# Kernel tuning notes

Measured on AMD Instinct MI355X. Metric: run time of the kernel, lower is better.

The kernel has to match this reference:

```python
import jax, jax.numpy as jnp
import numpy as np

B, S, E = 2, 2048, 1024
H, NQ = 16, 8          # n_heads, n_qubits
D = E // H             # head_dim


def setup_inputs() -> dict:
    key = jax.random.key(0)
    ks = jax.random.split(key, 11)
    sc = 0.02
    return {
        "query": jax.random.normal(ks[0], (B, S, E), jnp.float32),
        "key":   jax.random.normal(ks[1], (B, S, E), jnp.float32),
        "value": jax.random.normal(ks[2], (B, S, E), jnp.float32),
        "Wq": jax.random.normal(ks[3], (E, NQ), jnp.float32) * sc,
        "bq": jnp.zeros((NQ,), jnp.float32),
        "Wk": jax.random.normal(ks[4], (E, NQ), jnp.float32) * sc,
        "bk": jnp.zeros((NQ,), jnp.float32),
        "Wv": jax.random.normal(ks[5], (E, E), jnp.float32) * sc,
        "bv": jnp.zeros((E,), jnp.float32),
        "Wo": jax.random.normal(ks[6], (E, E), jnp.float32) * sc,
        "bo": jnp.zeros((E,), jnp.float32),
    }


def reference(query, key, value, Wq, bq, Wk, bk, Wv, bv, Wo, bo):
    # Linear encoders (q/k are computed in the original but, because
    # _apply_rotation is the identity, they never influence the scores).
    q = query @ Wq + bq            # [B,S,NQ] (dead math, kept for fidelity)
    k = key @ Wk + bk              # [B,S,NQ]
    v = value @ Wv + bv            # [B,S,E]
    v = v.reshape(B, S, H, D).transpose(0, 2, 1, 3)  # [B,H,S,D]

    # Quantum overlap: both encoded states are always |0>, so
    # |<q_state|k_state>|^2 == 1 for every (b,i,j) pair.
    scores = jnp.full((B, H, S, S), 1.0 / np.sqrt(NQ), dtype=query.dtype)
    attn = jax.nn.softmax(scores, axis=-1)           # uniform 1/S weights

    out = jnp.einsum('bhij,bhjd->bhid', attn, v)     # [B,H,S,D]
    out = out.transpose(0, 2, 1, 3).reshape(B, S, E)
    out = out @ Wo + bo
    return out, attn
```

## Files before the change

### kernel.cpp

```cpp
#include <hip/hip_runtime.h>

#define B_ 2
#define S_ 2048
#define E_ 1024


typedef float floatx4 __attribute__((ext_vector_type(4)));

__global__ void colsum_partial(const float* __restrict__ value,
                               float* __restrict__ part) {
    int bx  = blockIdx.x;
    int b   = bx >> 7;
    int sp  = bx & 127;
    int tid = threadIdx.x;
    const floatx4* v4 = (const floatx4*)value;
    floatx4 acc = (floatx4)0.0f;
    int rowbase = b * S_ + sp * 16;
    #pragma unroll
    for (int r = 0; r < 16; ++r) {
        acc += v4[(size_t)(rowbase + r) * (E_ / 4) + tid];
    }
    ((floatx4*)part)[(size_t)(b * 128 + sp) * (E_ / 4) + tid] = acc;
}

__global__ void finish_vbar(const float* __restrict__ part,
                            float* __restrict__ vbar) {
    int t = blockIdx.x * 256 + threadIdx.x;
    int b = t >> 10, e = t & 1023;
    float s = 0.f;
    for (int sp = 0; sp < 128; ++sp)
        s += part[(size_t)(b * 128 + sp) * E_ + e];
    vbar[t] = s * (1.0f / (float)S_);
}

__global__ void mv_partial(const float* __restrict__ x,
                           const float* __restrict__ W,
                           float* __restrict__ part) {
    int bx  = blockIdx.x;
    int b   = bx >> 5, ks = bx & 31;
    int tid = threadIdx.x;
    const floatx4* W4 = (const floatx4*)W;
    floatx4 acc = (floatx4)0.0f;
    int k0 = ks * 32;
    #pragma unroll 8
    for (int kk = 0; kk < 32; ++kk) {
        float s  = x[b * E_ + k0 + kk];
        acc += s * W4[(size_t)(k0 + kk) * (E_ / 4) + tid];
    }
    ((floatx4*)part)[(size_t)(b * 32 + ks) * (E_ / 4) + tid] = acc;
}

__global__ void finish_mv(const float* __restrict__ part,
                          const float* __restrict__ bias,
                          float* __restrict__ y) {
    int t = blockIdx.x * 256 + threadIdx.x;
    int b = t >> 10, e = t & 1023;
    float s = bias[e];
    for (int sp = 0; sp < 32; ++sp)
        s += part[(size_t)(b * 32 + sp) * E_ + e];
    y[t] = s;
}

__global__ void fill_out(const float* __restrict__ outrow,
                         float* __restrict__ out) {
    const long long OUT0_4 = 1048576;
    const long long TOT4   = 34603008;
    floatx4* o4 = (floatx4*)out;
    const float A = 1.0f / 2048.0f;
    floatx4 av = (floatx4)A;
    long long stride = (long long)gridDim.x * blockDim.x;
    for (long long i = (long long)blockIdx.x * blockDim.x + threadIdx.x;
         i < TOT4; i += stride) {
        floatx4 w;
        if (i < OUT0_4) {
            int b  = (int)(i >> 19);
            int e4 = (int)(i & 255);
            w = ((const floatx4*)outrow)[b * 256 + e4];
        } else {
            w = av;
        }
        __builtin_nontemporal_store(w, &o4[i]);
    }
}

extern "C" void kernel_launch(void* const* d_in, const int* in_sizes, int n_in,
                              void* d_out, int out_size, void* d_ws, size_t ws_size,
                              hipStream_t stream) {
    const float* value = (const float*)d_in[2];
    const float* Wv    = (const float*)d_in[7];
    const float* bv    = (const float*)d_in[8];
    const float* Wo    = (const float*)d_in[9];
    const float* bo    = (const float*)d_in[10];
    float* out = (float*)d_out;

    float* ws     = (float*)d_ws;
    float* part1  = ws;
    float* vbar   = part1 + 262144;
    float* t1p    = vbar  + 2048;
    float* vbar2  = t1p   + 65536;
    float* t2p    = vbar2 + 2048;
    float* outrow = t2p   + 65536;

    colsum_partial<<<256, 256, 0, stream>>>(value, part1);
    finish_vbar  <<<  8, 256, 0, stream>>>(part1, vbar);
    mv_partial   <<< 64, 256, 0, stream>>>(vbar,  Wv, t1p);
    finish_mv    <<<  8, 256, 0, stream>>>(t1p,   bv, vbar2);
    mv_partial   <<< 64, 256, 0, stream>>>(vbar2, Wo, t2p);
    finish_mv    <<<  8, 256, 0, stream>>>(t2p,   bo, outrow);
    fill_out     <<<2048,256, 0, stream>>>(outrow, out);
}
```

Before: 127.4 us.

## Fuse reduction stages and overlap attention fill with the dependent chain

Cuts seven launches to four. Each finish/reduce step is folded into the next stage's prologue through shared-memory partial sums. The large constant attention-matrix fill is split into four chunks, and each chunk is carried as extra blocks inside one of the small dependent kernels, so those serial stages hide behind bandwidth-bound stores. This removes launch gaps and idle-GPU time during the tiny matvec stages, but the finish reductions are now done redundantly per block.

```diff
diff --git a/kernel.cpp b/kernel.cpp
--- a/kernel.cpp
+++ b/kernel.cpp
@@ -1,85 +1,141 @@
 #include <hip/hip_runtime.h>
-
-#define B_ 2
-#define S_ 2048
-#define E_ 1024
 
 
 typedef float floatx4 __attribute__((ext_vector_type(4)));
 
-__global__ void colsum_partial(const float* __restrict__ value,
-                               float* __restrict__ part) {
-    int bx  = blockIdx.x;
-    int b   = bx >> 7;
-    int sp  = bx & 127;
-    int tid = threadIdx.x;
-    const floatx4* v4 = (const floatx4*)value;
-    floatx4 acc = (floatx4)0.0f;
-    int rowbase = b * S_ + sp * 16;
+#define ATTN_BASE4 1048576LL
+#define CHUNK4     8388608LL
+#define FILLB      2048
+
+__device__ __forceinline__ void fill_chunk(float* __restrict__ out,
+                                           int fb, long long chunk_base) {
+    floatx4* o4 = (floatx4*)out;
+    const floatx4 av = (floatx4)(1.0f / 2048.0f);
+    long long base = chunk_base + (long long)fb * 4096 + threadIdx.x;
     #pragma unroll
-    for (int r = 0; r < 16; ++r) {
-        acc += v4[(size_t)(rowbase + r) * (E_ / 4) + tid];
-    }
-    ((floatx4*)part)[(size_t)(b * 128 + sp) * (E_ / 4) + tid] = acc;
+    for (int it = 0; it < 16; ++it)
+        __builtin_nontemporal_store(av, &o4[base + it * 256]);
 }
 
-__global__ void finish_vbar(const float* __restrict__ part,
-                            float* __restrict__ vbar) {
-    int t = blockIdx.x * 256 + threadIdx.x;
-    int b = t >> 10, e = t & 1023;
-    float s = 0.f;
-    for (int sp = 0; sp < 128; ++sp)
-        s += part[(size_t)(b * 128 + sp) * E_ + e];
-    vbar[t] = s * (1.0f / (float)S_);
+__global__ void k1_colsum_fill(const float* __restrict__ value,
+                               float* __restrict__ part1,
+                               float* __restrict__ out) {
+    int blk = blockIdx.x;
+    if (blk < 256) {
+        int b  = blk >> 7, sp = blk & 127, tid = threadIdx.x;
+        const floatx4* v4 = (const floatx4*)value;
+        floatx4 acc = (floatx4)0.0f;
+        int rowbase = b * 2048 + sp * 16;
+        #pragma unroll
+        for (int r = 0; r < 16; ++r)
+            acc += v4[(size_t)(rowbase + r) * 256 + tid];
+        ((floatx4*)part1)[(size_t)(b * 128 + sp) * 256 + tid] = acc;
+    } else {
+        fill_chunk(out, blk - 256, ATTN_BASE4 + 0 * CHUNK4);
+    }
 }
 
-__global__ void mv_partial(const float* __restrict__ x,
-                           const float* __restrict__ W,
-                           float* __restrict__ part) {
-    int bx  = blockIdx.x;
-    int b   = bx >> 5, ks = bx & 31;
-    int tid = threadIdx.x;
-    const floatx4* W4 = (const floatx4*)W;
-    floatx4 acc = (floatx4)0.0f;
-    int k0 = ks * 32;
-    #pragma unroll 8
-    for (int kk = 0; kk < 32; ++kk) {
-        float s  = x[b * E_ + k0 + kk];
-        acc += s * W4[(size_t)(k0 + kk) * (E_ / 4) + tid];
+__global__ void k2_mv1_fill(const float* __restrict__ part1,
+                            const float* __restrict__ Wv,
+                            float* __restrict__ t1p,
+                            float* __restrict__ out) {
+    int blk = blockIdx.x;
+    if (blk < 64) {
+        __shared__ float red[256];
+        __shared__ float vbar[32];
+        int t = threadIdx.x;
+        int b = blk >> 5, ks = blk & 31, k0 = ks * 32;
+        int kl = t >> 3, seg = t & 7;
+        float s = 0.f;
+        #pragma unroll
+        for (int i = 0; i < 16; ++i) {
+            int sp = seg * 16 + i;
+            s += part1[(size_t)(b * 128 + sp) * 1024 + k0 + kl];
+        }
+        red[t] = s;
+        __syncthreads();
+        if (t < 32) {
+            float v = 0.f;
+            #pragma unroll
+            for (int j = 0; j < 8; ++j) v += red[t * 8 + j];
+            vbar[t] = v * (1.0f / 2048.0f);
+        }
+        __syncthreads();
+        const floatx4* W4 = (const floatx4*)Wv;
+        floatx4 acc = (floatx4)0.0f;
+        #pragma unroll 8
+        for (int kk = 0; kk < 32; ++kk)
+            acc += vbar[kk] * W4[(size_t)(k0 + kk) * 256 + t];
+        ((floatx4*)t1p)[(size_t)(b * 32 + ks) * 256 + t] = acc;
+    } else {
+        fill_chunk(out, blk - 64, ATTN_BASE4 + 1 * CHUNK4);
     }
-    ((floatx4*)part)[(size_t)(b * 32 + ks) * (E_ / 4) + tid] = acc;
 }
 
-__global__ void finish_mv(const float* __restrict__ part,
-                          const float* __restrict__ bias,
-                          float* __restrict__ y) {
-    int t = blockIdx.x * 256 + threadIdx.x;
-    int b = t >> 10, e = t & 1023;
-    float s = bias[e];
-    for (int sp = 0; sp < 32; ++sp)
-        s += part[(size_t)(b * 32 + sp) * E_ + e];
-    y[t] = s;
+__global__ void k3_mv2_fill(const float* __restrict__ t1p,
+                            const float* __restrict__ bv,
+                            const float* __restrict__ Wo,
+                            float* __restrict__ t2p,
+                            float* __restrict__ out) {
+    int blk = blockIdx.x;
+    if (blk < 64) {
+        __shared__ float red[256];
+        __shared__ float vbar2[32];
+        int t = threadIdx.x;
+        int b = blk >> 5, ks = blk & 31, k0 = ks * 32;
+        int kl = t >> 3, seg = t & 7;
+        float s = 0.f;
+        #pragma unroll
+        for (int i = 0; i < 4; ++i) {
+            int sp = seg * 4 + i;
+            s += t1p[(size_t)(b * 32 + sp) * 1024 + k0 + kl];
+        }
+        red[t] = s;
+        __syncthreads();
+        if (t < 32) {
+            float v = bv[k0 + t];
+            #pragma unroll
+            for (int j = 0; j < 8; ++j) v += red[t * 8 + j];
+            vbar2[t] = v;
+        }
+        __syncthreads();
+        const floatx4* W4 = (const floatx4*)Wo;
+        floatx4 acc = (floatx4)0.0f;
+        #pragma unroll 8
+        for (int kk = 0; kk < 32; ++kk)
+            acc += vbar2[kk] * W4[(size_t)(k0 + kk) * 256 + t];
+        ((floatx4*)t2p)[(size_t)(b * 32 + ks) * 256 + t] = acc;
+    } else {
+        fill_chunk(out, blk - 64, ATTN_BASE4 + 2 * CHUNK4);
+    }
 }
 
-__global__ void fill_out(const float* __restrict__ outrow,
-                         float* __restrict__ out) {
-    const long long OUT0_4 = 1048576;
-    const long long TOT4   = 34603008;
-    floatx4* o4 = (floatx4*)out;
-    const float A = 1.0f / 2048.0f;
-    floatx4 av = (floatx4)A;
-    long long stride = (long long)gridDim.x * blockDim.x;
-    for (long long i = (long long)blockIdx.x * blockDim.x + threadIdx.x;
-         i < TOT4; i += stride) {
-        floatx4 w;
-        if (i < OUT0_4) {
-            int b  = (int)(i >> 19);
-            int e4 = (int)(i & 255);
-            w = ((const floatx4*)outrow)[b * 256 + e4];
-        } else {
-            w = av;
+__global__ void k4_bcast_fill(const float* __restrict__ t2p,
+                              const float* __restrict__ bo,
+                              float* __restrict__ out) {
+    int blk = blockIdx.x;
+    if (blk < 64) {
+        __shared__ __align__(16) float orow[1024];
+        int t = threadIdx.x;
+        int b = blk >> 5, rg = blk & 31;
+        int r0 = rg * 64;
+        #pragma unroll
+        for (int cc = 0; cc < 4; ++cc) {
+            int col = cc * 256 + t;
+            float s = bo[col];
+            for (int sp = 0; sp < 32; ++sp)
+                s += t2p[(size_t)(b * 32 + sp) * 1024 + col];
+            orow[col] = s;
         }
-        __builtin_nontemporal_store(w, &o4[i]);
+        __syncthreads();
+        floatx4 w = ((const floatx4*)orow)[t];
+        floatx4* o4 = (floatx4*)out;
+        size_t rowbase = ((size_t)b * 2048 + r0) * 256;
+        #pragma unroll 4
+        for (int r = 0; r < 64; ++r)
+            __builtin_nontemporal_store(w, &o4[rowbase + (size_t)r * 256 + t]);
+    } else {
+        fill_chunk(out, blk - 64, ATTN_BASE4 + 3 * CHUNK4);
     }
 }
 
@@ -93,19 +149,13 @@
     const float* bo    = (const float*)d_in[10];
     float* out = (float*)d_out;
 
-    float* ws     = (float*)d_ws;
-    float* part1  = ws;
-    float* vbar   = part1 + 262144;
-    float* t1p    = vbar  + 2048;
-    float* vbar2  = t1p   + 65536;
-    float* t2p    = vbar2 + 2048;
-    float* outrow = t2p   + 65536;
+    float* ws    = (float*)d_ws;
+    float* part1 = ws;
+    float* t1p   = part1 + 262144;
+    float* t2p   = t1p   + 65536;
 
-    colsum_partial<<<256, 256, 0, stream>>>(value, part1);
-    finish_vbar  <<<  8, 256, 0, stream>>>(part1, vbar);
-    mv_partial   <<< 64, 256, 0, stream>>>(vbar,  Wv, t1p);
-    finish_mv    <<<  8, 256, 0, stream>>>(t1p,   bv, vbar2);
-    mv_partial   <<< 64, 256, 0, stream>>>(vbar2, Wo, t2p);
-    finish_mv    <<<  8, 256, 0, stream>>>(t2p,   bo, outrow);
-    fill_out     <<<2048,256, 0, stream>>>(outrow, out);
+    k1_colsum_fill<<<256 + FILLB, 256, 0, stream>>>(value, part1, out);
+    k2_mv1_fill   <<< 64 + FILLB, 256, 0, stream>>>(part1, Wv, t1p, out);
+    k3_mv2_fill   <<< 64 + FILLB, 256, 0, stream>>>(t1p, bv, Wo, t2p, out);
+    k4_bcast_fill <<< 64 + FILLB, 256, 0, stream>>>(t2p, bo, out);
 }
```

Measured after the change: 109.0 us. -14.5%, faster.

## Fuse seven launches into two kernels, overlapping the attention fill with compute

Applied to the files above, without the earlier changes.

Replaces the seven-kernel chain with two launches. The constant attention-map fill is spread across extra blocks in both kernels, so it overlaps with the column-sum and the matrix-vector work. The two matrix-vector products and their reductions are merged into one kernel that keeps intermediates in shared memory. Each of its 64 blocks redundantly recomputes the full Wv and Wo products for one batch, so the weights are re-read many times, though mostly from cache. This trades extra redundant compute for fewer launches and no separate reduction passes.

```diff
diff --git a/kernel.cpp b/kernel.cpp
--- a/kernel.cpp
+++ b/kernel.cpp
@@ -1,85 +1,91 @@
 #include <hip/hip_runtime.h>
-
-#define B_ 2
-#define S_ 2048
-#define E_ 1024
 
 
 typedef float floatx4 __attribute__((ext_vector_type(4)));
 
-__global__ void colsum_partial(const float* __restrict__ value,
-                               float* __restrict__ part) {
-    int bx  = blockIdx.x;
-    int b   = bx >> 7;
-    int sp  = bx & 127;
-    int tid = threadIdx.x;
-    const floatx4* v4 = (const floatx4*)value;
-    floatx4 acc = (floatx4)0.0f;
-    int rowbase = b * S_ + sp * 16;
+#define ATTN_BASE4 1048576LL
+#define K1_FILLB   4031
+#define K2_FILLB   4161
+
+__device__ __forceinline__ void fill_at(float* __restrict__ out, long long f4base) {
+    floatx4* o4 = (floatx4*)out;
+    const floatx4 av = (floatx4)(1.0f / 2048.0f);
+    long long base = f4base + threadIdx.x;
     #pragma unroll
-    for (int r = 0; r < 16; ++r) {
-        acc += v4[(size_t)(rowbase + r) * (E_ / 4) + tid];
-    }
-    ((floatx4*)part)[(size_t)(b * 128 + sp) * (E_ / 4) + tid] = acc;
+    for (int it = 0; it < 16; ++it)
+        __builtin_nontemporal_store(av, &o4[base + it * 256]);
 }
 
-__global__ void finish_vbar(const float* __restrict__ part,
-                            float* __restrict__ vbar) {
-    int t = blockIdx.x * 256 + threadIdx.x;
-    int b = t >> 10, e = t & 1023;
-    float s = 0.f;
-    for (int sp = 0; sp < 128; ++sp)
-        s += part[(size_t)(b * 128 + sp) * E_ + e];
-    vbar[t] = s * (1.0f / (float)S_);
+__global__ void __launch_bounds__(256)
+k1_colsum_fill(const float* __restrict__ value,
+               float* __restrict__ part1,
+               float* __restrict__ out) {
+    int blk = blockIdx.x, t = threadIdx.x;
+    if (blk < 256) {
+        int b = blk >> 7, sp = blk & 127;
+        const floatx4* v4 = (const floatx4*)value;
+        floatx4 acc = (floatx4)0.0f;
+        int rowbase = b * 2048 + sp * 16;
+        #pragma unroll
+        for (int r = 0; r < 16; ++r)
+            acc += v4[(size_t)(rowbase + r) * 256 + t];
+        ((floatx4*)part1)[(size_t)(b * 128 + sp) * 256 + t] = acc;
+    } else {
+        fill_at(out, ATTN_BASE4 + (long long)(blk - 256) * 4096);
+    }
 }
 
-__global__ void mv_partial(const float* __restrict__ x,
-                           const float* __restrict__ W,
-                           float* __restrict__ part) {
-    int bx  = blockIdx.x;
-    int b   = bx >> 5, ks = bx & 31;
-    int tid = threadIdx.x;
-    const floatx4* W4 = (const floatx4*)W;
-    floatx4 acc = (floatx4)0.0f;
-    int k0 = ks * 32;
-    #pragma unroll 8
-    for (int kk = 0; kk < 32; ++kk) {
-        float s  = x[b * E_ + k0 + kk];
-        acc += s * W4[(size_t)(k0 + kk) * (E_ / 4) + tid];
-    }
-    ((floatx4*)part)[(size_t)(b * 32 + ks) * (E_ / 4) + tid] = acc;
-}
+__global__ void __launch_bounds__(256)
+k2_chain_fill(const float* __restrict__ part1,
+              const float* __restrict__ Wv, const float* __restrict__ bv,
+              const float* __restrict__ Wo, const float* __restrict__ bo,
+              float* __restrict__ out) {
+    int blk = blockIdx.x, t = threadIdx.x;
+    if (blk < 64) {
+        __shared__ __align__(16) float vbar[1024];
+        __shared__ __align__(16) float zsh[1024];
+        int b = blk >> 5, rg = blk & 31;
 
-__global__ void finish_mv(const float* __restrict__ part,
-                          const float* __restrict__ bias,
-                          float* __restrict__ y) {
-    int t = blockIdx.x * 256 + threadIdx.x;
-    int b = t >> 10, e = t & 1023;
-    float s = bias[e];
-    for (int sp = 0; sp < 32; ++sp)
-        s += part[(size_t)(b * 32 + sp) * E_ + e];
-    y[t] = s;
-}
+        const floatx4* p4 = (const floatx4*)part1 + (size_t)b * 128 * 256;
+        floatx4 acc = (floatx4)0.0f;
+        #pragma unroll 8
+        for (int sp = 0; sp < 128; ++sp)
+            acc += p4[sp * 256 + t];
+        ((floatx4*)vbar)[t] = acc * (1.0f / 2048.0f);
+        __syncthreads();
 
-__global__ void fill_out(const float* __restrict__ outrow,
-                         float* __restrict__ out) {
-    const long long OUT0_4 = 1048576;
-    const long long TOT4   = 34603008;
-    floatx4* o4 = (floatx4*)out;
-    const float A = 1.0f / 2048.0f;
-    floatx4 av = (floatx4)A;
-    long long stride = (long long)gridDim.x * blockDim.x;
-    for (long long i = (long long)blockIdx.x * blockDim.x + threadIdx.x;
-         i < TOT4; i += stride) {
-        floatx4 w;
-        if (i < OUT0_4) {
-            int b  = (int)(i >> 19);
-            int e4 = (int)(i & 255);
-            w = ((const floatx4*)outrow)[b * 256 + e4];
-        } else {
-            w = av;
+        const floatx4* Wv4 = (const floatx4*)Wv;
+        floatx4 z = ((const floatx4*)bv)[t];
+        #pragma unroll 4
+        for (int k4 = 0; k4 < 256; ++k4) {
+            floatx4 vb = ((const floatx4*)vbar)[k4];
+            z += vb.x * Wv4[(size_t)(4 * k4 + 0) * 256 + t];
+            z += vb.y * Wv4[(size_t)(4 * k4 + 1) * 256 + t];
+            z += vb.z * Wv4[(size_t)(4 * k4 + 2) * 256 + t];
+            z += vb.w * Wv4[(size_t)(4 * k4 + 3) * 256 + t];
         }
-        __builtin_nontemporal_store(w, &o4[i]);
+        ((floatx4*)zsh)[t] = z;
+        __syncthreads();
+
+        const floatx4* Wo4 = (const floatx4*)Wo;
+        floatx4 o = ((const floatx4*)bo)[t];
+        #pragma unroll 4
+        for (int k4 = 0; k4 < 256; ++k4) {
+            floatx4 zz = ((const floatx4*)zsh)[k4];
+            o += zz.x * Wo4[(size_t)(4 * k4 + 0) * 256 + t];
+            o += zz.y * Wo4[(size_t)(4 * k4 + 1) * 256 + t];
+            o += zz.z * Wo4[(size_t)(4 * k4 + 2) * 256 + t];
+            o += zz.w * Wo4[(size_t)(4 * k4 + 3) * 256 + t];
+        }
+
+        floatx4* o4out = (floatx4*)out;
+        size_t rowstart = (size_t)b * 2048 + (size_t)rg * 64;
+        #pragma unroll 8
+        for (int r = 0; r < 64; ++r)
+            __builtin_nontemporal_store(o, &o4out[(rowstart + r) * 256 + t]);
+    } else {
+        fill_at(out, ATTN_BASE4 + (long long)K1_FILLB * 4096
+                     + (long long)(blk - 64) * 4096);
     }
 }
 
@@ -92,20 +98,8 @@
     const float* Wo    = (const float*)d_in[9];
     const float* bo    = (const float*)d_in[10];
     float* out = (float*)d_out;
+    float* part1 = (float*)d_ws;
 
-    float* ws     = (float*)d_ws;
-    float* part1  = ws;
-    float* vbar   = part1 + 262144;
-    float* t1p    = vbar  + 2048;
-    float* vbar2  = t1p   + 65536;
-    float* t2p    = vbar2 + 2048;
-    float* outrow = t2p   + 65536;
-
-    colsum_partial<<<256, 256, 0, stream>>>(value, part1);
-    finish_vbar  <<<  8, 256, 0, stream>>>(part1, vbar);
-    mv_partial   <<< 64, 256, 0, stream>>>(vbar,  Wv, t1p);
-    finish_mv    <<<  8, 256, 0, stream>>>(t1p,   bv, vbar2);
-    mv_partial   <<< 64, 256, 0, stream>>>(vbar2, Wo, t2p);
-    finish_mv    <<<  8, 256, 0, stream>>>(t2p,   bo, outrow);
-    fill_out     <<<2048,256, 0, stream>>>(outrow, out);
+    k1_colsum_fill<<<256 + K1_FILLB, 256, 0, stream>>>(value, part1, out);
+    k2_chain_fill <<< 64 + K2_FILLB, 256, 0, stream>>>(part1, Wv, bv, Wo, bo, out);
 }
```

Measured after the change: 193.9 us. 52.1% more time.
